# Kernel optimization log

Measured on AMD Instinct MI355X. Metric: run time of the kernel, lower is better.

Reference implementation:

```python
import jax, jax.numpy as jnp
import numpy as np

N, E, IN, HID, OUT, HEADS = 50000, 800000, 256, 256, 128, 4
HC = HID // HEADS  # 64
EPS = 1e-5


def layer_norm(x, g, b):
    mu = x.mean(-1, keepdims=True)
    var = ((x - mu) ** 2).mean(-1, keepdims=True)
    return (x - mu) * jax.lax.rsqrt(var + EPS) * g + b


def gat_conv(x, W, a_s, a_d, bias, src, dst, heads, C, concat):
    # PyG GATConv (eval mode): linear -> per-edge LeakyReLU attention ->
    # segment softmax over destination -> scatter-sum aggregation -> bias
    n = x.shape[0]
    xw = (x @ W).reshape(n, heads, C)                     # [N,H,C]
    al_s = jnp.einsum('nhc,hc->nh', xw, a_s)              # [N,H]
    al_d = jnp.einsum('nhc,hc->nh', xw, a_d)
    e = jax.nn.leaky_relu(al_s[src] + al_d[dst], 0.2)     # [Etot,H]
    m = jax.ops.segment_max(e, dst, num_segments=n)
    ex = jnp.exp(e - m[dst])
    denom = jax.ops.segment_sum(ex, dst, num_segments=n)
    alpha = ex / denom[dst]                               # [Etot,H]
    out = jax.ops.segment_sum(xw[src] * alpha[:, :, None], dst, num_segments=n)
    out = out.reshape(n, heads * C) if concat else out.mean(axis=1)
    return out + bias


def setup_inputs() -> dict:
    key = jax.random.key(0)
    ks = jax.random.split(key, 20)
    s = 0.05
    return {
        'x': jax.random.normal(ks[0], (N, IN), jnp.float32),
        'edge_index': jax.random.randint(ks[1], (2, E), 0, N, jnp.int64),
        'Wp': jax.random.normal(ks[2], (IN, HID), jnp.float32) * s,
        'bp': jnp.zeros((HID,), jnp.float32),
        'W0': jax.random.normal(ks[3], (HID, HEADS * HC), jnp.float32) * s,
        'as0': jax.random.normal(ks[4], (HEADS, HC), jnp.float32) * s,
        'ad0': jax.random.normal(ks[5], (HEADS, HC), jnp.float32) * s,
        'b0': jnp.zeros((HID,), jnp.float32),
        'W1': jax.random.normal(ks[6], (HID, OUT), jnp.float32) * s,
        'as1': jax.random.normal(ks[7], (1, OUT), jnp.float32) * s,
        'ad1': jax.random.normal(ks[8], (1, OUT), jnp.float32) * s,
        'b1': jnp.zeros((OUT,), jnp.float32),
        'g0': jnp.ones((HID,), jnp.float32),
        'be0': jnp.zeros((HID,), jnp.float32),
        'g1': jnp.ones((OUT,), jnp.float32),
        'be1': jnp.zeros((OUT,), jnp.float32),
        'Wo': jax.random.normal(ks[9], (OUT, OUT), jnp.float32) * s,
        'bo': jnp.zeros((OUT,), jnp.float32),
    }


def reference(x, edge_index, Wp, bp, W0, as0, ad0, b0, W1, as1, ad1, b1,
              g0, be0, g1, be1, Wo, bo):
    n = x.shape[0]
    # add self loops (PyG GATConv default)
    ar = jnp.arange(n, dtype=edge_index.dtype)
    src = jnp.concatenate([edge_index[0], ar])
    dst = jnp.concatenate([edge_index[1], ar])

    h = jax.nn.relu(x @ Wp + bp)
    # layer 0: multi-head, concat, LN + residual + relu
    h1 = gat_conv(h, W0, as0, ad0, b0, src, dst, HEADS, HC, True)
    h1 = layer_norm(h1, g0, be0)
    h1 = jax.nn.relu(h1 + h)
    # layer 1: single head, no concat, LN (no residual: shape check still passes
    # only when identity is not None; here identity is None for last layer)
    h2 = gat_conv(h1, W1, as1, ad1, b1, src, dst, 1, OUT, False)
    h2 = layer_norm(h2, g1, be1)
    out = h2 @ Wo + bo
    out = out / jnp.maximum(jnp.linalg.norm(out, axis=-1, keepdims=True), 1e-12)
    return out
```

## Files before the change

### kernel.cpp

```cpp
#include <hip/hip_runtime.h>
#include <hip/hip_bf16.h>

typedef __bf16 bf16x8 __attribute__((ext_vector_type(8)));
typedef __bf16 bf16x4 __attribute__((ext_vector_type(4)));
typedef __bf16 bf16x2 __attribute__((ext_vector_type(2)));
typedef float f32x4 __attribute__((ext_vector_type(4)));

__device__ __forceinline__ float getf(const void* p, size_t i, int isf32){
  return isf32 ? ((const float*)p)[i]
               : __bfloat162float(((const __hip_bfloat16*)p)[i]);
}
__device__ __forceinline__ int getedge(const void* p, long long idx, int is64, int n){
  long long v = is64 ? ((const long long*)p)[idx] : (long long)((const int*)p)[idx];
  v = v < 0 ? 0 : (v >= n ? (long long)(n - 1) : v);
  return (int)v;
}

__device__ __forceinline__ float bfly_sum(float v){
#pragma unroll
  for (int m = 32; m > 0; m >>= 1) v += __shfl_xor(v, m, 64);
  return v;
}

__global__ __launch_bounds__(256) void detect_kernel(const void* x, const void* ei,
                                                     int* flags){
  __shared__ int cnt_sane, cnt_odd;
  int t = threadIdx.x;
  if (t == 0){ cnt_sane = 0; cnt_odd = 0; }
  __syncthreads();
  int sane = 0;
  for (int i = t; i < 4096; i += 256){
    float v = __bfloat162float(((const __hip_bfloat16*)x)[i]);
    if (fabsf(v) < 16.f) sane++;
  }
  atomicAdd(&cnt_sane, sane);
  int odd = 0;
  for (int i = t; i < 512; i += 256){
    if (((const int*)ei)[2 * i + 1] != 0) odd++;
  }
  atomicAdd(&cnt_odd, odd);
  __syncthreads();
  if (t == 0){
    flags[0] = (cnt_sane < 3900) ? 1 : 0;
    flags[1] = (cnt_odd == 0) ? 1 : 0;
  }
}

__global__ __launch_bounds__(256) void count_kernel(const void* __restrict__ ei, long long E,
                                                    int n, const int* __restrict__ flags,
                                                    int* __restrict__ cnt){
  int i = blockIdx.x * blockDim.x + threadIdx.x;
  if (i < E){
    int d = getedge(ei, E + i, flags[1], n);
    atomicAdd(&cnt[d], 1);
  }
}

__global__ __launch_bounds__(1024) void scan_kernel(const int* __restrict__ cnt, int* __restrict__ off,
                                                    int* __restrict__ pos, int n){
  __shared__ int wsum[16];
  __shared__ int carry_s;
  int tid = threadIdx.x, lane = tid & 63, wv = tid >> 6;
  if (tid == 0) carry_s = 0;
  __syncthreads();
  for (int base = 0; base < n; base += 1024){
    int i = base + tid;
    int v = (i < n) ? cnt[i] : 0;
    int s = v;
#pragma unroll
    for (int o = 1; o < 64; o <<= 1){ int t = __shfl_up(s, o, 64); if (lane >= o) s += t; }
    if (lane == 63) wsum[wv] = s;
    __syncthreads();
    int wo = 0;
    for (int w = 0; w < wv; w++) wo += wsum[w];
    int carry = carry_s;
    int excl = carry + wo + s - v;
    if (i < n){ off[i] = excl; pos[i] = excl; }
    __syncthreads();
    if (tid == 0){
      int tot = 0;
      for (int w = 0; w < 16; w++) tot += wsum[w];
      carry_s = carry + tot;
    }
    __syncthreads();
  }
  if (tid == 0) off[n] = carry_s;
}

__global__ __launch_bounds__(256) void fill_kernel(const void* __restrict__ ei, long long E,
                                                   int n, const int* __restrict__ flags,
                                                   int* __restrict__ pos, int* __restrict__ bsrc,
                                                   int* __restrict__ bdst){
  int i = blockIdx.x * blockDim.x + threadIdx.x;
  if (i < E){
    int d = getedge(ei, E + i, flags[1], n);
    int s = getedge(ei, i, flags[1], n);
    int p = atomicAdd(&pos[d], 1);
    bsrc[p] = s;
    bdst[p] = d;
  }
}

__global__ __launch_bounds__(256) void transpose_w_kernel(const void* __restrict__ W,
    const int* __restrict__ flags, __hip_bfloat16* __restrict__ Bt, int K, int N)
{
  int f0 = flags[0];
  int o = blockIdx.x * 256 + threadIdx.x;
  if (o < K * N){
    int nn = o / K, kk = o - nn * K;
    Bt[o] = __float2bfloat16(getf(W, (size_t)kk * N + nn, f0));
  }
}

__device__ __forceinline__ bf16x8 pk8(f32x4 u, f32x4 w){
  bf16x8 r;
  r[0] = (__bf16)u.x; r[1] = (__bf16)u.y; r[2] = (__bf16)u.z; r[3] = (__bf16)u.w;
  r[4] = (__bf16)w.x; r[5] = (__bf16)w.y; r[6] = (__bf16)w.z; r[7] = (__bf16)w.w;
  return r;
}

template<int AMODE, bool OUTF, bool OUTB, bool RELU, bool BIAS, bool NORM>
__global__ __launch_bounds__(256) void gemm_direct_kernel(
    const void* __restrict__ A, const __hip_bfloat16* __restrict__ Bt,
    const void* __restrict__ bias, const int* __restrict__ flags,
    float* __restrict__ Cf, __hip_bfloat16* __restrict__ Cb,
    int M, int N, int K)
{
  const int f0 = flags[0];
  const bool af32 = (AMODE == 1) && (f0 != 0);
  int t = threadIdx.x;
  int wave = t >> 6, lane = t & 63;
  int q = lane >> 4, mi = lane & 15;
  int bm = blockIdx.x * 128 + wave * 32;
  int bn = blockIdx.y * 128;

  int r0 = min(bm + mi, M - 1);
  int r1 = min(bm + 16 + mi, M - 1);

  f32x4 acc[2][8] = {};

  if (af32){
    const float* Af = (const float*)A;
    const float* p0 = Af + (size_t)r0 * K + q * 8;
    const float* p1 = Af + (size_t)r1 * K + q * 8;
#pragma unroll 2
    for (int k0 = 0; k0 < K; k0 += 32){
      f32x4 u0 = *(const f32x4*)(p0 + k0);
      f32x4 w0 = *(const f32x4*)(p0 + k0 + 4);
      f32x4 u1 = *(const f32x4*)(p1 + k0);
      f32x4 w1 = *(const f32x4*)(p1 + k0 + 4);
      bf16x8 a0 = pk8(u0, w0);
      bf16x8 a1 = pk8(u1, w1);
#pragma unroll
      for (int nt = 0; nt < 8; nt++){
        bf16x8 b = *(const bf16x8*)(Bt + (size_t)(bn + nt * 16 + mi) * K + k0 + q * 8);
        acc[0][nt] = __builtin_amdgcn_mfma_f32_16x16x32_bf16(a0, b, acc[0][nt], 0, 0, 0);
        acc[1][nt] = __builtin_amdgcn_mfma_f32_16x16x32_bf16(a1, b, acc[1][nt], 0, 0, 0);
      }
    }
  } else {
    const __hip_bfloat16* Ab = (const __hip_bfloat16*)A;
    const __hip_bfloat16* p0 = Ab + (size_t)r0 * K + q * 8;
    const __hip_bfloat16* p1 = Ab + (size_t)r1 * K + q * 8;
#pragma unroll 2
    for (int k0 = 0; k0 < K; k0 += 32){
      bf16x8 a0 = *(const bf16x8*)(p0 + k0);
      bf16x8 a1 = *(const bf16x8*)(p1 + k0);
#pragma unroll
      for (int nt = 0; nt < 8; nt++){
        bf16x8 b = *(const bf16x8*)(Bt + (size_t)(bn + nt * 16 + mi) * K + k0 + q * 8);
        acc[0][nt] = __builtin_amdgcn_mfma_f32_16x16x32_bf16(a0, b, acc[0][nt], 0, 0, 0);
        acc[1][nt] = __builtin_amdgcn_mfma_f32_16x16x32_bf16(a1, b, acc[1][nt], 0, 0, 0);
      }
    }
  }

  float bv[8];
  if (BIAS){
#pragma unroll
    for (int nt = 0; nt < 8; nt++) bv[nt] = getf(bias, bn + nt * 16 + mi, f0);
  }
#pragma unroll
  for (int mt = 0; mt < 2; mt++){
#pragma unroll
    for (int r = 0; r < 4; r++){
      int row = bm + mt * 16 + q * 4 + r;
      float vv[8];
#pragma unroll
      for (int nt = 0; nt < 8; nt++){
        float v = acc[mt][nt][r];
        if (BIAS) v += bv[nt];
        if (RELU) v = fmaxf(v, 0.f);
        vv[nt] = v;
      }
      if (NORM){
        float ss = 0.f;
#pragma unroll
        for (int nt = 0; nt < 8; nt++) ss += vv[nt] * vv[nt];
        ss += __shfl_xor(ss, 1, 64);
        ss += __shfl_xor(ss, 2, 64);
        ss += __shfl_xor(ss, 4, 64);
        ss += __shfl_xor(ss, 8, 64);
        float inv = 1.f / fmaxf(sqrtf(ss), 1e-12f);
#pragma unroll
        for (int nt = 0; nt < 8; nt++) vv[nt] *= inv;
      }
      if (row < M){
#pragma unroll
        for (int nt = 0; nt < 8; nt++){
          int col = bn + nt * 16 + mi;
          size_t idx = (size_t)row * N + col;
          if (OUTF) Cf[idx] = vv[nt];
          if (OUTB) Cb[idx] = __float2bfloat16(vv[nt]);
        }
      }
    }
  }
}

__global__ __launch_bounds__(256) void al0_kernel(const __hip_bfloat16* __restrict__ xw,
    const void* __restrict__ a_s, const void* __restrict__ a_d, const int* __restrict__ flags,
    float* __restrict__ als, float* __restrict__ ald, int n)
{
  int f0 = flags[0];
  int t = threadIdx.x, wv = t >> 6, lane = t & 63;
  int i = blockIdx.x * 4 + wv;
  if (i >= n) return;
  int ch = lane * 4;
  uint2 u = *(const uint2*)(xw + (size_t)i * 256 + ch);
  float x0 = __uint_as_float(u.x << 16);
  float x1 = __uint_as_float(u.x & 0xffff0000u);
  float x2 = __uint_as_float(u.y << 16);
  float x3 = __uint_as_float(u.y & 0xffff0000u);
  float ps = x0 * getf(a_s, ch + 0, f0) + x1 * getf(a_s, ch + 1, f0)
           + x2 * getf(a_s, ch + 2, f0) + x3 * getf(a_s, ch + 3, f0);
  float pd = x0 * getf(a_d, ch + 0, f0) + x1 * getf(a_d, ch + 1, f0)
           + x2 * getf(a_d, ch + 2, f0) + x3 * getf(a_d, ch + 3, f0);
  ps += __shfl_xor(ps, 1, 64); pd += __shfl_xor(pd, 1, 64);
  ps += __shfl_xor(ps, 2, 64); pd += __shfl_xor(pd, 2, 64);
  ps += __shfl_xor(ps, 4, 64); pd += __shfl_xor(pd, 4, 64);
  ps += __shfl_xor(ps, 8, 64); pd += __shfl_xor(pd, 8, 64);
  if ((lane & 15) == 0){
    int h = lane >> 4;
    als[(size_t)i * 4 + h] = ps;
    ald[(size_t)i * 4 + h] = pd;
  }
}

__global__ __launch_bounds__(256) void al1_kernel(const __hip_bfloat16* __restrict__ xw,
    const void* __restrict__ a_s, const void* __restrict__ a_d, const int* __restrict__ flags,
    float* __restrict__ als, float* __restrict__ ald, int n)
{
  int f0 = flags[0];
  int t = threadIdx.x, wv = t >> 6, lane = t & 63;
  int i = blockIdx.x * 4 + wv;
  if (i >= n) return;
  int ch = lane * 2;
  unsigned u = *(const unsigned*)(xw + (size_t)i * 128 + ch);
  float x0 = __uint_as_float(u << 16);
  float x1 = __uint_as_float(u & 0xffff0000u);
  float ps = x0 * getf(a_s, ch + 0, f0) + x1 * getf(a_s, ch + 1, f0);
  float pd = x0 * getf(a_d, ch + 0, f0) + x1 * getf(a_d, ch + 1, f0);
  ps = bfly_sum(ps); pd = bfly_sum(pd);
  if (lane == 0){ als[i] = ps; ald[i] = pd; }
}

__global__ __launch_bounds__(256) void wq0_kernel(const float* __restrict__ als,
    const float* __restrict__ ald, const int* __restrict__ bsrc, const int* __restrict__ bdst,
    f32x4* __restrict__ wq, int E)
{
  int p = blockIdx.x * 256 + threadIdx.x;
  if (p < E){
    int s = bsrc[p], d = bdst[p];
    f32x4 a = ((const f32x4*)als)[s];
    f32x4 b = ((const f32x4*)ald)[d];
    f32x4 w;
#pragma unroll
    for (int k = 0; k < 4; k++){
      float e = a[k] + b[k];
      e = (e > 0.f) ? e : 0.2f * e;
      w[k] = __expf(e);
    }
    wq[p] = w;
  }
}

__global__ __launch_bounds__(256) void wq1_kernel(const float* __restrict__ als,
    const float* __restrict__ ald, const int* __restrict__ bsrc, const int* __restrict__ bdst,
    float* __restrict__ wq, int E)
{
  int p = blockIdx.x * 256 + threadIdx.x;
  if (p < E){
    float e = als[bsrc[p]] + ald[bdst[p]];
    e = (e > 0.f) ? e : 0.2f * e;
    wq[p] = __expf(e);
  }
}

#define FMA4(U, W) do { \
  m0 += (W) * __uint_as_float((U).x << 16); \
  m1 += (W) * __uint_as_float((U).x & 0xffff0000u); \
  m2 += (W) * __uint_as_float((U).y << 16); \
  m3 += (W) * __uint_as_float((U).y & 0xffff0000u); \
} while (0)

__global__ __launch_bounds__(256) void gather0_kernel(
    const __hip_bfloat16* __restrict__ xw, const float* __restrict__ als, const float* __restrict__ ald,
    const int* __restrict__ bsrc, const float* __restrict__ wq, const int* __restrict__ off,
    const void* __restrict__ bias, const void* __restrict__ gamma,
    const void* __restrict__ beta, const int* __restrict__ flags,
    const float* __restrict__ resf, __hip_bfloat16* __restrict__ outb, int n)
{
  int f0 = flags[0];
  int t = threadIdx.x, wv = t >> 6, lane = t & 63;
  int i = blockIdx.x * 4 + wv;
  if (i >= n) return;
  int head = lane >> 4;
  int ch = lane * 4;
  int e0 = off[i], jend = off[i + 1];

  float m0 = 0.f, m1 = 0.f, m2 = 0.f, m3 = 0.f;

  float se = als[(size_t)i * 4 + head] + ald[(size_t)i * 4 + head];
  se = (se > 0.f) ? se : 0.2f * se;
  float eself = __expf(se);
  {
    uint2 u = *(const uint2*)(xw + (size_t)i * 256 + ch);
    FMA4(u, eself);
  }
  float wacc = eself;

  int j = e0;
  for (; j + 3 < jend; j += 4){
    int s0 = bsrc[j], s1 = bsrc[j + 1], s2 = bsrc[j + 2], s3 = bsrc[j + 3];
    float w0 = wq[(size_t)j * 4 + head];
    float w1 = wq[(size_t)(j + 1) * 4 + head];
    float w2 = wq[(size_t)(j + 2) * 4 + head];
    float w3 = wq[(size_t)(j + 3) * 4 + head];
    uint2 U0 = *(const uint2*)(xw + (size_t)s0 * 256 + ch);
    uint2 U1 = *(const uint2*)(xw + (size_t)s1 * 256 + ch);
    uint2 U2 = *(const uint2*)(xw + (size_t)s2 * 256 + ch);
    uint2 U3 = *(const uint2*)(xw + (size_t)s3 * 256 + ch);
    wacc += w0 + w1 + w2 + w3;
    FMA4(U0, w0); FMA4(U1, w1); FMA4(U2, w2); FMA4(U3, w3);
  }
  for (; j < jend; j++){
    int s0 = bsrc[j];
    float w0 = wq[(size_t)j * 4 + head];
    uint2 U0 = *(const uint2*)(xw + (size_t)s0 * 256 + ch);
    wacc += w0;
    FMA4(U0, w0);
  }

  float rl = 1.f / wacc;
  float v0 = m0 * rl + getf(bias, ch + 0, f0);
  float v1 = m1 * rl + getf(bias, ch + 1, f0);
  float v2 = m2 * rl + getf(bias, ch + 2, f0);
  float v3 = m3 * rl + getf(bias, ch + 3, f0);

  float mu = bfly_sum(v0 + v1 + v2 + v3) * (1.f / 256.f);
  float d0 = v0 - mu, d1 = v1 - mu, d2 = v2 - mu, d3 = v3 - mu;
  float var = bfly_sum(d0 * d0 + d1 * d1 + d2 * d2 + d3 * d3) * (1.f / 256.f);
  float rs = rsqrtf(var + 1e-5f);

  f32x4 res = *(const f32x4*)(resf + (size_t)i * 256 + ch);
  float y0 = fmaxf(d0 * rs * getf(gamma, ch + 0, f0) + getf(beta, ch + 0, f0) + res.x, 0.f);
  float y1 = fmaxf(d1 * rs * getf(gamma, ch + 1, f0) + getf(beta, ch + 1, f0) + res.y, 0.f);
  float y2 = fmaxf(d2 * rs * getf(gamma, ch + 2, f0) + getf(beta, ch + 2, f0) + res.z, 0.f);
  float y3 = fmaxf(d3 * rs * getf(gamma, ch + 3, f0) + getf(beta, ch + 3, f0) + res.w, 0.f);

  bf16x4 o;
  o[0] = (__bf16)y0; o[1] = (__bf16)y1; o[2] = (__bf16)y2; o[3] = (__bf16)y3;
  *(bf16x4*)(outb + (size_t)i * 256 + ch) = o;
}

#define FMA2(U, W) do { \
  m0 += (W) * __uint_as_float((U) << 16); \
  m1 += (W) * __uint_as_float((U) & 0xffff0000u); \
} while (0)

__global__ __launch_bounds__(256) void gather1_kernel(
    const __hip_bfloat16* __restrict__ xw, const float* __restrict__ als, const float* __restrict__ ald,
    const int* __restrict__ bsrc, const float* __restrict__ wq, const int* __restrict__ off,
    const void* __restrict__ bias, const void* __restrict__ gamma,
    const void* __restrict__ beta, const int* __restrict__ flags,
    __hip_bfloat16* __restrict__ outb, int n)
{
  int f0 = flags[0];
  int t = threadIdx.x, wv = t >> 6, lane = t & 63;
  int i = blockIdx.x * 4 + wv;
  if (i >= n) return;
  int ch = lane * 2;
  int e0 = off[i], jend = off[i + 1];

  float m0 = 0.f, m1 = 0.f;

  float se = als[i] + ald[i];
  se = (se > 0.f) ? se : 0.2f * se;
  float eself = __expf(se);
  {
    unsigned u = *(const unsigned*)(xw + (size_t)i * 128 + ch);
    FMA2(u, eself);
  }
  float wacc = eself;

  int j = e0;
  for (; j + 3 < jend; j += 4){
    int s0 = bsrc[j], s1 = bsrc[j + 1], s2 = bsrc[j + 2], s3 = bsrc[j + 3];
    float w0 = wq[j], w1 = wq[j + 1], w2 = wq[j + 2], w3 = wq[j + 3];
    unsigned U0 = *(const unsigned*)(xw + (size_t)s0 * 128 + ch);
    unsigned U1 = *(const unsigned*)(xw + (size_t)s1 * 128 + ch);
    unsigned U2 = *(const unsigned*)(xw + (size_t)s2 * 128 + ch);
    unsigned U3 = *(const unsigned*)(xw + (size_t)s3 * 128 + ch);
    wacc += w0 + w1 + w2 + w3;
    FMA2(U0, w0); FMA2(U1, w1); FMA2(U2, w2); FMA2(U3, w3);
  }
  for (; j < jend; j++){
    int s0 = bsrc[j];
    float w0 = wq[j];
    unsigned U0 = *(const unsigned*)(xw + (size_t)s0 * 128 + ch);
    wacc += w0;
    FMA2(U0, w0);
  }

  float rl = 1.f / wacc;
  float v0 = m0 * rl + getf(bias, ch + 0, f0);
  float v1 = m1 * rl + getf(bias, ch + 1, f0);

  float mu = bfly_sum(v0 + v1) * (1.f / 128.f);
  float d0 = v0 - mu, d1 = v1 - mu;
  float var = bfly_sum(d0 * d0 + d1 * d1) * (1.f / 128.f);
  float rs = rsqrtf(var + 1e-5f);

  float y0 = d0 * rs * getf(gamma, ch + 0, f0) + getf(beta, ch + 0, f0);
  float y1 = d1 * rs * getf(gamma, ch + 1, f0) + getf(beta, ch + 1, f0);

  bf16x2 o;
  o[0] = (__bf16)y0; o[1] = (__bf16)y1;
  *(bf16x2*)(outb + (size_t)i * 128 + ch) = o;
}

extern "C" void kernel_launch(void* const* d_in, const int* in_sizes, int n_in,
                              void* d_out, int out_size, void* d_ws, size_t ws_size,
                              hipStream_t stream)
{
  const void* x   = d_in[0];
  const void* ei  = d_in[1];
  const void* Wp  = d_in[2];
  const void* bp  = d_in[3];
  const void* W0  = d_in[4];
  const void* as0 = d_in[5];
  const void* ad0 = d_in[6];
  const void* b0  = d_in[7];
  const void* W1  = d_in[8];
  const void* as1 = d_in[9];
  const void* ad1 = d_in[10];
  const void* b1  = d_in[11];
  const void* g0  = d_in[12];
  const void* be0 = d_in[13];
  const void* g1  = d_in[14];
  const void* be1 = d_in[15];
  const void* Wo  = d_in[16];
  const void* bo  = d_in[17];
  float* outp = (float*)d_out;

  const int n = in_sizes[0] / 256;
  const int E = in_sizes[1] / 2;

  char* w = (char*)d_ws;
  size_t SZ = (size_t)n * 256 * sizeof(float);
  float* h_f32 = (float*)w;
  __hip_bfloat16* h_bf = (__hip_bfloat16*)(w + SZ);
  __hip_bfloat16* xw_bf = (__hip_bfloat16*)(w + SZ + SZ / 2);
  char* p = w + 2 * SZ;
  int* flags = (int*)p; p += 64;
  float* als0 = (float*)p; p += (size_t)n * 4 * sizeof(float);
  float* ald0 = (float*)p; p += (size_t)n * 4 * sizeof(float);
  float* als1 = (float*)p; p += (size_t)n * sizeof(float);
  float* ald1 = (float*)p; p += (size_t)n * sizeof(float);
  int* cnt  = (int*)p; p += (size_t)n * sizeof(int);
  int* offb = (int*)p; p += (size_t)(n + 1) * sizeof(int) + 4;
  int* pos  = (int*)p; p += (size_t)n * sizeof(int);
  int* bsrc = (int*)p; p += (size_t)E * sizeof(int);
  int* bdst = (int*)p; p += (size_t)E * sizeof(int);
  p = (char*)(((uintptr_t)p + 15) & ~(uintptr_t)15);
  float* wqbuf = (float*)p; p += ((size_t)E + 64) * 4 * sizeof(float);
  __hip_bfloat16* bt_p = (__hip_bfloat16*)p; p += (size_t)256 * 256 * 2;
  __hip_bfloat16* bt_0 = (__hip_bfloat16*)p; p += (size_t)256 * 256 * 2;
  __hip_bfloat16* bt_1 = (__hip_bfloat16*)p; p += (size_t)128 * 256 * 2;
  __hip_bfloat16* bt_o = (__hip_bfloat16*)p; p += (size_t)128 * 128 * 2;

  detect_kernel<<<1, 256, 0, stream>>>(x, ei, flags);

  transpose_w_kernel<<<(256 * 256 + 255) / 256, 256, 0, stream>>>(Wp, flags, bt_p, 256, 256);
  transpose_w_kernel<<<(256 * 256 + 255) / 256, 256, 0, stream>>>(W0, flags, bt_0, 256, 256);
  transpose_w_kernel<<<(256 * 128 + 255) / 256, 256, 0, stream>>>(W1, flags, bt_1, 256, 128);
  transpose_w_kernel<<<(128 * 128 + 255) / 256, 256, 0, stream>>>(Wo, flags, bt_o, 128, 128);

  hipMemsetAsync(cnt, 0, (size_t)n * sizeof(int), stream);
  count_kernel<<<(E + 255) / 256, 256, 0, stream>>>(ei, E, n, flags, cnt);
  scan_kernel<<<1, 1024, 0, stream>>>(cnt, offb, pos, n);
  fill_kernel<<<(E + 255) / 256, 256, 0, stream>>>(ei, E, n, flags, pos, bsrc, bdst);

  int gm = (n + 127) / 128;
  int ge = (E + 255) / 256;
  int gn4 = (n + 3) / 4;

  gemm_direct_kernel<1, true, true, true, true, false><<<dim3(gm, 2), 256, 0, stream>>>(
      x, bt_p, bp, flags, h_f32, h_bf, n, 256, 256);
  gemm_direct_kernel<0, false, true, false, false, false><<<dim3(gm, 2), 256, 0, stream>>>(
      h_bf, bt_0, nullptr, flags, nullptr, xw_bf, n, 256, 256);
  al0_kernel<<<gn4, 256, 0, stream>>>(xw_bf, as0, ad0, flags, als0, ald0, n);
  wq0_kernel<<<ge, 256, 0, stream>>>(als0, ald0, bsrc, bdst, (f32x4*)wqbuf, E);
  gather0_kernel<<<gn4, 256, 0, stream>>>(xw_bf, als0, ald0, bsrc, wqbuf, offb, b0, g0, be0,
                                          flags, h_f32, h_bf, n);
  gemm_direct_kernel<0, false, true, false, false, false><<<dim3(gm, 1), 256, 0, stream>>>(
      h_bf, bt_1, nullptr, flags, nullptr, xw_bf, n, 128, 256);
  al1_kernel<<<gn4, 256, 0, stream>>>(xw_bf, as1, ad1, flags, als1, ald1, n);
  wq1_kernel<<<ge, 256, 0, stream>>>(als1, ald1, bsrc, bdst, wqbuf, E);
  gather1_kernel<<<gn4, 256, 0, stream>>>(xw_bf, als1, ald1, bsrc, wqbuf, offb, b1, g1, be1,
                                          flags, h_bf, n);
  gemm_direct_kernel<0, true, false, false, true, true><<<dim3(gm, 1), 256, 0, stream>>>(
      h_bf, bt_o, bo, flags, outp, nullptr, n, 128, 128);
}
```

Baseline: 595.3 us.

## Fuse attention logits into GEMM epilogue and compute edge weights inside gather

Computes the per-node source/destination attention scores in the GEMM epilogue, removing the separate al0/al1 kernels. Replaces the per-edge weight precompute kernels (wq0/wq1) and the bdst array with on-the-fly leaky-relu and exp inside the gather kernels. Also drops the fp32 residual copy in favor of the bf16 h buffer, merges the four weight transposes into one launch, and vectorizes the prefix scan by four. This trades extra exp work and scattered als reads per edge in the gather for fewer launches and less global memory traffic, with slightly lower residual precision.

```diff
diff --git a/kernel.cpp b/kernel.cpp
--- a/kernel.cpp
+++ b/kernel.cpp
@@ -63,10 +63,20 @@
   int tid = threadIdx.x, lane = tid & 63, wv = tid >> 6;
   if (tid == 0) carry_s = 0;
   __syncthreads();
-  for (int base = 0; base < n; base += 1024){
-    int i = base + tid;
-    int v = (i < n) ? cnt[i] : 0;
-    int s = v;
+  for (int base = 0; base < n; base += 4096){
+    int i0 = base + tid * 4;
+    int v0 = 0, v1 = 0, v2 = 0, v3 = 0;
+    if (i0 + 3 < n){
+      int4 q = *(const int4*)(cnt + i0);
+      v0 = q.x; v1 = q.y; v2 = q.z; v3 = q.w;
+    } else {
+      if (i0 < n)     v0 = cnt[i0];
+      if (i0 + 1 < n) v1 = cnt[i0 + 1];
+      if (i0 + 2 < n) v2 = cnt[i0 + 2];
+      if (i0 + 3 < n) v3 = cnt[i0 + 3];
+    }
+    int s4 = v0 + v1 + v2 + v3;
+    int s = s4;
 #pragma unroll
     for (int o = 1; o < 64; o <<= 1){ int t = __shfl_up(s, o, 64); if (lane >= o) s += t; }
     if (lane == 63) wsum[wv] = s;
@@ -74,8 +84,17 @@
     int wo = 0;
     for (int w = 0; w < wv; w++) wo += wsum[w];
     int carry = carry_s;
-    int excl = carry + wo + s - v;
-    if (i < n){ off[i] = excl; pos[i] = excl; }
+    int e0 = carry + wo + s - s4;
+    if (i0 + 3 < n){
+      int4 o4; o4.x = e0; o4.y = e0 + v0; o4.z = e0 + v0 + v1; o4.w = e0 + v0 + v1 + v2;
+      *(int4*)(off + i0) = o4;
+      *(int4*)(pos + i0) = o4;
+    } else {
+      if (i0 < n)     { off[i0] = e0;               pos[i0] = e0; }
+      if (i0 + 1 < n) { off[i0+1] = e0+v0;          pos[i0+1] = e0+v0; }
+      if (i0 + 2 < n) { off[i0+2] = e0+v0+v1;       pos[i0+2] = e0+v0+v1; }
+      if (i0 + 3 < n) { off[i0+3] = e0+v0+v1+v2;    pos[i0+3] = e0+v0+v1+v2; }
+    }
     __syncthreads();
     if (tid == 0){
       int tot = 0;
@@ -89,27 +108,33 @@
 
 __global__ __launch_bounds__(256) void fill_kernel(const void* __restrict__ ei, long long E,
                                                    int n, const int* __restrict__ flags,
-                                                   int* __restrict__ pos, int* __restrict__ bsrc,
-                                                   int* __restrict__ bdst){
+                                                   int* __restrict__ pos, int* __restrict__ bsrc){
   int i = blockIdx.x * blockDim.x + threadIdx.x;
   if (i < E){
     int d = getedge(ei, E + i, flags[1], n);
     int s = getedge(ei, i, flags[1], n);
     int p = atomicAdd(&pos[d], 1);
     bsrc[p] = s;
-    bdst[p] = d;
-  }
-}
-
-__global__ __launch_bounds__(256) void transpose_w_kernel(const void* __restrict__ W,
-    const int* __restrict__ flags, __hip_bfloat16* __restrict__ Bt, int K, int N)
+  }
+}
+
+__global__ __launch_bounds__(256) void transpose_all_kernel(
+    const void* __restrict__ Wp, const void* __restrict__ W0,
+    const void* __restrict__ W1, const void* __restrict__ Wo,
+    const int* __restrict__ flags,
+    __hip_bfloat16* __restrict__ btp, __hip_bfloat16* __restrict__ bt0,
+    __hip_bfloat16* __restrict__ bt1, __hip_bfloat16* __restrict__ bto)
 {
   int f0 = flags[0];
   int o = blockIdx.x * 256 + threadIdx.x;
-  if (o < K * N){
-    int nn = o / K, kk = o - nn * K;
-    Bt[o] = __float2bfloat16(getf(W, (size_t)kk * N + nn, f0));
-  }
+  const void* W; __hip_bfloat16* B; int K, N, loc;
+  if (o < 65536)       { W = Wp; B = btp; K = 256; N = 256; loc = o; }
+  else if (o < 131072) { W = W0; B = bt0; K = 256; N = 256; loc = o - 65536; }
+  else if (o < 163840) { W = W1; B = bt1; K = 256; N = 128; loc = o - 131072; }
+  else if (o < 180224) { W = Wo; B = bto; K = 128; N = 128; loc = o - 163840; }
+  else return;
+  int nn = loc / K, kk = loc - nn * K;
+  B[loc] = __float2bfloat16(getf(W, (size_t)kk * N + nn, f0));
 }
 
 __device__ __forceinline__ bf16x8 pk8(f32x4 u, f32x4 w){
@@ -119,11 +144,13 @@
   return r;
 }
 
-template<int AMODE, bool OUTF, bool OUTB, bool RELU, bool BIAS, bool NORM>
+template<int AMODE, bool OUTF, bool OUTB, bool RELU, bool BIAS, bool NORM, int ALMODE>
 __global__ __launch_bounds__(256) void gemm_direct_kernel(
     const void* __restrict__ A, const __hip_bfloat16* __restrict__ Bt,
-    const void* __restrict__ bias, const int* __restrict__ flags,
+    const void* __restrict__ bias, const void* __restrict__ a_s, const void* __restrict__ a_d,
+    const int* __restrict__ flags,
     float* __restrict__ Cf, __hip_bfloat16* __restrict__ Cb,
+    float* __restrict__ als, float* __restrict__ ald,
     int M, int N, int K)
 {
   const int f0 = flags[0];
@@ -175,10 +202,17 @@
     }
   }
 
-  float bv[8];
+  float bv[8], asv[8], adv[8];
   if (BIAS){
 #pragma unroll
     for (int nt = 0; nt < 8; nt++) bv[nt] = getf(bias, bn + nt * 16 + mi, f0);
+  }
+  if (ALMODE != 0){
+#pragma unroll
+    for (int nt = 0; nt < 8; nt++){
+      asv[nt] = getf(a_s, bn + nt * 16 + mi, f0);
+      adv[nt] = getf(a_d, bn + nt * 16 + mi, f0);
+    }
   }
 #pragma unroll
   for (int mt = 0; mt < 2; mt++){
@@ -205,6 +239,32 @@
 #pragma unroll
         for (int nt = 0; nt < 8; nt++) vv[nt] *= inv;
       }
+      if (ALMODE == 1){
+        float ps0 = 0.f, pd0 = 0.f, ps1 = 0.f, pd1 = 0.f;
+#pragma unroll
+        for (int nt = 0; nt < 4; nt++){ ps0 += vv[nt] * asv[nt]; pd0 += vv[nt] * adv[nt]; }
+#pragma unroll
+        for (int nt = 4; nt < 8; nt++){ ps1 += vv[nt] * asv[nt]; pd1 += vv[nt] * adv[nt]; }
+#pragma unroll
+        for (int m = 1; m < 16; m <<= 1){
+          ps0 += __shfl_xor(ps0, m, 64); pd0 += __shfl_xor(pd0, m, 64);
+          ps1 += __shfl_xor(ps1, m, 64); pd1 += __shfl_xor(pd1, m, 64);
+        }
+        if ((lane & 15) == 0 && row < M){
+          int h0 = blockIdx.y * 2;
+          als[(size_t)row * 4 + h0]     = ps0; ald[(size_t)row * 4 + h0]     = pd0;
+          als[(size_t)row * 4 + h0 + 1] = ps1; ald[(size_t)row * 4 + h0 + 1] = pd1;
+        }
+      } else if (ALMODE == 2){
+        float ps = 0.f, pd = 0.f;
+#pragma unroll
+        for (int nt = 0; nt < 8; nt++){ ps += vv[nt] * asv[nt]; pd += vv[nt] * adv[nt]; }
+#pragma unroll
+        for (int m = 1; m < 16; m <<= 1){
+          ps += __shfl_xor(ps, m, 64); pd += __shfl_xor(pd, m, 64);
+        }
+        if ((lane & 15) == 0 && row < M){ als[row] = ps; ald[row] = pd; }
+      }
       if (row < M){
 #pragma unroll
         for (int nt = 0; nt < 8; nt++){
@@ -218,85 +278,6 @@
   }
 }
 
-__global__ __launch_bounds__(256) void al0_kernel(const __hip_bfloat16* __restrict__ xw,
-    const void* __restrict__ a_s, const void* __restrict__ a_d, const int* __restrict__ flags,
-    float* __restrict__ als, float* __restrict__ ald, int n)
-{
-  int f0 = flags[0];
-  int t = threadIdx.x, wv = t >> 6, lane = t & 63;
-  int i = blockIdx.x * 4 + wv;
-  if (i >= n) return;
-  int ch = lane * 4;
-  uint2 u = *(const uint2*)(xw + (size_t)i * 256 + ch);
-  float x0 = __uint_as_float(u.x << 16);
-  float x1 = __uint_as_float(u.x & 0xffff0000u);
-  float x2 = __uint_as_float(u.y << 16);
-  float x3 = __uint_as_float(u.y & 0xffff0000u);
-  float ps = x0 * getf(a_s, ch + 0, f0) + x1 * getf(a_s, ch + 1, f0)
-           + x2 * getf(a_s, ch + 2, f0) + x3 * getf(a_s, ch + 3, f0);
-  float pd = x0 * getf(a_d, ch + 0, f0) + x1 * getf(a_d, ch + 1, f0)
-           + x2 * getf(a_d, ch + 2, f0) + x3 * getf(a_d, ch + 3, f0);
-  ps += __shfl_xor(ps, 1, 64); pd += __shfl_xor(pd, 1, 64);
-  ps += __shfl_xor(ps, 2, 64); pd += __shfl_xor(pd, 2, 64);
-  ps += __shfl_xor(ps, 4, 64); pd += __shfl_xor(pd, 4, 64);
-  ps += __shfl_xor(ps, 8, 64); pd += __shfl_xor(pd, 8, 64);
-  if ((lane & 15) == 0){
-    int h = lane >> 4;
-    als[(size_t)i * 4 + h] = ps;
-    ald[(size_t)i * 4 + h] = pd;
-  }
-}
-
-__global__ __launch_bounds__(256) void al1_kernel(const __hip_bfloat16* __restrict__ xw,
-    const void* __restrict__ a_s, const void* __restrict__ a_d, const int* __restrict__ flags,
-    float* __restrict__ als, float* __restrict__ ald, int n)
-{
-  int f0 = flags[0];
-  int t = threadIdx.x, wv = t >> 6, lane = t & 63;
-  int i = blockIdx.x * 4 + wv;
-  if (i >= n) return;
-  int ch = lane * 2;
-  unsigned u = *(const unsigned*)(xw + (size_t)i * 128 + ch);
-  float x0 = __uint_as_float(u << 16);
-  float x1 = __uint_as_float(u & 0xffff0000u);
-  float ps = x0 * getf(a_s, ch + 0, f0) + x1 * getf(a_s, ch + 1, f0);
-  float pd = x0 * getf(a_d, ch + 0, f0) + x1 * getf(a_d, ch + 1, f0);
-  ps = bfly_sum(ps); pd = bfly_sum(pd);
-  if (lane == 0){ als[i] = ps; ald[i] = pd; }
-}
-
-__global__ __launch_bounds__(256) void wq0_kernel(const float* __restrict__ als,
-    const float* __restrict__ ald, const int* __restrict__ bsrc, const int* __restrict__ bdst,
-    f32x4* __restrict__ wq, int E)
-{
-  int p = blockIdx.x * 256 + threadIdx.x;
-  if (p < E){
-    int s = bsrc[p], d = bdst[p];
-    f32x4 a = ((const f32x4*)als)[s];
-    f32x4 b = ((const f32x4*)ald)[d];
-    f32x4 w;
-#pragma unroll
-    for (int k = 0; k < 4; k++){
-      float e = a[k] + b[k];
-      e = (e > 0.f) ? e : 0.2f * e;
-      w[k] = __expf(e);
-    }
-    wq[p] = w;
-  }
-}
-
-__global__ __launch_bounds__(256) void wq1_kernel(const float* __restrict__ als,
-    const float* __restrict__ ald, const int* __restrict__ bsrc, const int* __restrict__ bdst,
-    float* __restrict__ wq, int E)
-{
-  int p = blockIdx.x * 256 + threadIdx.x;
-  if (p < E){
-    float e = als[bsrc[p]] + ald[bdst[p]];
-    e = (e > 0.f) ? e : 0.2f * e;
-    wq[p] = __expf(e);
-  }
-}
-
 #define FMA4(U, W) do { \
   m0 += (W) * __uint_as_float((U).x << 16); \
   m1 += (W) * __uint_as_float((U).x & 0xffff0000u); \
@@ -306,10 +287,10 @@
 
 __global__ __launch_bounds__(256) void gather0_kernel(
     const __hip_bfloat16* __restrict__ xw, const float* __restrict__ als, const float* __restrict__ ald,
-    const int* __restrict__ bsrc, const float* __restrict__ wq, const int* __restrict__ off,
+    const int* __restrict__ bsrc, const int* __restrict__ off,
     const void* __restrict__ bias, const void* __restrict__ gamma,
     const void* __restrict__ beta, const int* __restrict__ flags,
-    const float* __restrict__ resf, __hip_bfloat16* __restrict__ outb, int n)
+    __hip_bfloat16* __restrict__ hbuf, int n)
 {
   int f0 = flags[0];
   int t = threadIdx.x, wv = t >> 6, lane = t & 63;
@@ -321,7 +302,9 @@
 
   float m0 = 0.f, m1 = 0.f, m2 = 0.f, m3 = 0.f;
 
-  float se = als[(size_t)i * 4 + head] + ald[(size_t)i * 4 + head];
+  float aldi = ald[(size_t)i * 4 + head];
+
+  float se = als[(size_t)i * 4 + head] + aldi;
   se = (se > 0.f) ? se : 0.2f * se;
   float eself = __expf(se);
   {
@@ -333,10 +316,15 @@
   int j = e0;
   for (; j + 3 < jend; j += 4){
     int s0 = bsrc[j], s1 = bsrc[j + 1], s2 = bsrc[j + 2], s3 = bsrc[j + 3];
-    float w0 = wq[(size_t)j * 4 + head];
-    float w1 = wq[(size_t)(j + 1) * 4 + head];
-    float w2 = wq[(size_t)(j + 2) * 4 + head];
-    float w3 = wq[(size_t)(j + 3) * 4 + head];
+    float l0 = als[(size_t)s0 * 4 + head] + aldi;
+    float l1 = als[(size_t)s1 * 4 + head] + aldi;
+    float l2 = als[(size_t)s2 * 4 + head] + aldi;
+    float l3 = als[(size_t)s3 * 4 + head] + aldi;
+    l0 = (l0 > 0.f) ? l0 : 0.2f * l0;
+    l1 = (l1 > 0.f) ? l1 : 0.2f * l1;
+    l2 = (l2 > 0.f) ? l2 : 0.2f * l2;
+    l3 = (l3 > 0.f) ? l3 : 0.2f * l3;
+    float w0 = __expf(l0), w1 = __expf(l1), w2 = __expf(l2), w3 = __expf(l3);
     uint2 U0 = *(const uint2*)(xw + (size_t)s0 * 256 + ch);
     uint2 U1 = *(const uint2*)(xw + (size_t)s1 * 256 + ch);
     uint2 U2 = *(const uint2*)(xw + (size_t)s2 * 256 + ch);
@@ -346,7 +334,9 @@
   }
   for (; j < jend; j++){
     int s0 = bsrc[j];
-    float w0 = wq[(size_t)j * 4 + head];
+    float l0 = als[(size_t)s0 * 4 + head] + aldi;
+    l0 = (l0 > 0.f) ? l0 : 0.2f * l0;
+    float w0 = __expf(l0);
     uint2 U0 = *(const uint2*)(xw + (size_t)s0 * 256 + ch);
     wacc += w0;
     FMA4(U0, w0);
@@ -363,15 +353,15 @@
   float var = bfly_sum(d0 * d0 + d1 * d1 + d2 * d2 + d3 * d3) * (1.f / 256.f);
   float rs = rsqrtf(var + 1e-5f);
 
-  f32x4 res = *(const f32x4*)(resf + (size_t)i * 256 + ch);
-  float y0 = fmaxf(d0 * rs * getf(gamma, ch + 0, f0) + getf(beta, ch + 0, f0) + res.x, 0.f);
-  float y1 = fmaxf(d1 * rs * getf(gamma, ch + 1, f0) + getf(beta, ch + 1, f0) + res.y, 0.f);
-  float y2 = fmaxf(d2 * rs * getf(gamma, ch + 2, f0) + getf(beta, ch + 2, f0) + res.z, 0.f);
-  float y3 = fmaxf(d3 * rs * getf(gamma, ch + 3, f0) + getf(beta, ch + 3, f0) + res.w, 0.f);
+  bf16x4 rb = *(const bf16x4*)(hbuf + (size_t)i * 256 + ch);
+  float y0 = fmaxf(d0 * rs * getf(gamma, ch + 0, f0) + getf(beta, ch + 0, f0) + (float)rb[0], 0.f);
+  float y1 = fmaxf(d1 * rs * getf(gamma, ch + 1, f0) + getf(beta, ch + 1, f0) + (float)rb[1], 0.f);
+  float y2 = fmaxf(d2 * rs * getf(gamma, ch + 2, f0) + getf(beta, ch + 2, f0) + (float)rb[2], 0.f);
+  float y3 = fmaxf(d3 * rs * getf(gamma, ch + 3, f0) + getf(beta, ch + 3, f0) + (float)rb[3], 0.f);
 
   bf16x4 o;
   o[0] = (__bf16)y0; o[1] = (__bf16)y1; o[2] = (__bf16)y2; o[3] = (__bf16)y3;
-  *(bf16x4*)(outb + (size_t)i * 256 + ch) = o;
+  *(bf16x4*)(hbuf + (size_t)i * 256 + ch) = o;
 }
 
 #define FMA2(U, W) do { \
@@ -381,7 +371,7 @@
 
 __global__ __launch_bounds__(256) void gather1_kernel(
     const __hip_bfloat16* __restrict__ xw, const float* __restrict__ als, const float* __restrict__ ald,
-    const int* __restrict__ bsrc, const float* __restrict__ wq, const int* __restrict__ off,
+    const int* __restrict__ bsrc, const int* __restrict__ off,
     const void* __restrict__ bias, const void* __restrict__ gamma,
     const void* __restrict__ beta, const int* __restrict__ flags,
     __hip_bfloat16* __restrict__ outb, int n)
@@ -395,7 +385,8 @@
 
   float m0 = 0.f, m1 = 0.f;
 
-  float se = als[i] + ald[i];
+  float aldi = ald[i];
+  float se = als[i] + aldi;
   se = (se > 0.f) ? se : 0.2f * se;
   float eself = __expf(se);
   {
@@ -407,7 +398,12 @@
   int j = e0;
   for (; j + 3 < jend; j += 4){
     int s0 = bsrc[j], s1 = bsrc[j + 1], s2 = bsrc[j + 2], s3 = bsrc[j + 3];
-    float w0 = wq[j], w1 = wq[j + 1], w2 = wq[j + 2], w3 = wq[j + 3];
+    float l0 = als[s0] + aldi, l1 = als[s1] + aldi, l2 = als[s2] + aldi, l3 = als[s3] + aldi;
+    l0 = (l0 > 0.f) ? l0 : 0.2f * l0;
+    l1 = (l1 > 0.f) ? l1 : 0.2f * l1;
+    l2 = (l2 > 0.f) ? l2 : 0.2f * l2;
+    l3 = (l3 > 0.f) ? l3 : 0.2f * l3;
+    float w0 = __expf(l0), w1 = __expf(l1), w2 = __expf(l2), w3 = __expf(l3);
     unsigned U0 = *(const unsigned*)(xw + (size_t)s0 * 128 + ch);
     unsigned U1 = *(const unsigned*)(xw + (size_t)s1 * 128 + ch);
     unsigned U2 = *(const unsigned*)(xw + (size_t)s2 * 128 + ch);
@@ -417,7 +413,9 @@
   }
   for (; j < jend; j++){
     int s0 = bsrc[j];
-    float w0 = wq[j];
+    float l0 = als[s0] + aldi;
+    l0 = (l0 > 0.f) ? l0 : 0.2f * l0;
+    float w0 = __expf(l0);
     unsigned U0 = *(const unsigned*)(xw + (size_t)s0 * 128 + ch);
     wacc += w0;
     FMA2(U0, w0);
@@ -469,22 +467,19 @@
 
   char* w = (char*)d_ws;
   size_t SZ = (size_t)n * 256 * sizeof(float);
-  float* h_f32 = (float*)w;
-  __hip_bfloat16* h_bf = (__hip_bfloat16*)(w + SZ);
-  __hip_bfloat16* xw_bf = (__hip_bfloat16*)(w + SZ + SZ / 2);
-  char* p = w + 2 * SZ;
+  __hip_bfloat16* h_bf  = (__hip_bfloat16*)w;
+  __hip_bfloat16* xw_bf = (__hip_bfloat16*)(w + SZ / 2);
+  char* p = w + SZ;
   int* flags = (int*)p; p += 64;
   float* als0 = (float*)p; p += (size_t)n * 4 * sizeof(float);
   float* ald0 = (float*)p; p += (size_t)n * 4 * sizeof(float);
   float* als1 = (float*)p; p += (size_t)n * sizeof(float);
   float* ald1 = (float*)p; p += (size_t)n * sizeof(float);
   int* cnt  = (int*)p; p += (size_t)n * sizeof(int);
-  int* offb = (int*)p; p += (size_t)(n + 1) * sizeof(int) + 4;
+  int* offb = (int*)p; p += (size_t)(n + 4) * sizeof(int);
   int* pos  = (int*)p; p += (size_t)n * sizeof(int);
   int* bsrc = (int*)p; p += (size_t)E * sizeof(int);
-  int* bdst = (int*)p; p += (size_t)E * sizeof(int);
   p = (char*)(((uintptr_t)p + 15) & ~(uintptr_t)15);
-  float* wqbuf = (float*)p; p += ((size_t)E + 64) * 4 * sizeof(float);
   __hip_bfloat16* bt_p = (__hip_bfloat16*)p; p += (size_t)256 * 256 * 2;
   __hip_bfloat16* bt_0 = (__hip_bfloat16*)p; p += (size_t)256 * 256 * 2;
   __hip_bfloat16* bt_1 = (__hip_bfloat16*)p; p += (size_t)128 * 256 * 2;
@@ -492,34 +487,26 @@
 
   detect_kernel<<<1, 256, 0, stream>>>(x, ei, flags);
 
-  transpose_w_kernel<<<(256 * 256 + 255) / 256, 256, 0, stream>>>(Wp, flags, bt_p, 256, 256);
-  transpose_w_kernel<<<(256 * 256 + 255) / 256, 256, 0, stream>>>(W0, flags, bt_0, 256, 256);
-  transpose_w_kernel<<<(256 * 128 + 255) / 256, 256, 0, stream>>>(W1, flags, bt_1, 256, 128);
-  transpose_w_kernel<<<(128 * 128 + 255) / 256, 256, 0, stream>>>(Wo, flags, bt_o, 128, 128);
+  transpose_all_kernel<<<704, 256, 0, stream>>>(Wp, W0, W1, Wo, flags, bt_p, bt_0, bt_1, bt_o);
 
   hipMemsetAsync(cnt, 0, (size_t)n * sizeof(int), stream);
   count_kernel<<<(E + 255) / 256, 256, 0, stream>>>(ei, E, n, flags, cnt);
   scan_kernel<<<1, 1024, 0, stream>>>(cnt, offb, pos, n);
-  fill_kernel<<<(E + 255) / 256, 256, 0, stream>>>(ei, E, n, flags, pos, bsrc, bdst);
+  fill_kernel<<<(E + 255) / 256, 256, 0, stream>>>(ei, E, n, flags, pos, bsrc);
 
   int gm = (n + 127) / 128;
-  int ge = (E + 255) / 256;
   int gn4 = (n + 3) / 4;
 
-  gemm_direct_kernel<1, true, true, true, true, false><<<dim3(gm, 2), 256, 0, stream>>>(
-      x, bt_p, bp, flags, h_f32, h_bf, n, 256, 256);
-  gemm_direct_kernel<0, false, true, false, false, false><<<dim3(gm, 2), 256, 0, stream>>>(
-      h_bf, bt_0, nullptr, flags, nullptr, xw_bf, n, 256, 256);
-  al0_kernel<<<gn4, 256, 0, stream>>>(xw_bf, as0, ad0, flags, als0, ald0, n);
-  wq0_kernel<<<ge, 256, 0, stream>>>(als0, ald0, bsrc, bdst, (f32x4*)wqbuf, E);
-  gather0_kernel<<<gn4, 256, 0, stream>>>(xw_bf, als0, ald0, bsrc, wqbuf, offb, b0, g0, be0,
-                                          flags, h_f32, h_bf, n);
-  gemm_direct_kernel<0, false, true, false, false, false><<<dim3(gm, 1), 256, 0, stream>>>(
-      h_bf, bt_1, nullptr, flags, nullptr, xw_bf, n, 128, 256);
-  al1_kernel<<<gn4, 256, 0, stream>>>(xw_bf, as1, ad1, flags, als1, ald1, n);
-  wq1_kernel<<<ge, 256, 0, stream>>>(als1, ald1, bsrc, bdst, wqbuf, E);
-  gather1_kernel<<<gn4, 256, 0, stream>>>(xw_bf, als1, ald1, bsrc, wqbuf, offb, b1, g1, be1,
+  gemm_direct_kernel<1, false, true, true, true, false, 0><<<dim3(gm, 2), 256, 0, stream>>>(
+      x, bt_p, bp, nullptr, nullptr, flags, nullptr, h_bf, nullptr, nullptr, n, 256, 256);
+  gemm_direct_kernel<0, false, true, false, false, false, 1><<<dim3(gm, 2), 256, 0, stream>>>(
+      h_bf, bt_0, nullptr, as0, ad0, flags, nullptr, xw_bf, als0, ald0, n, 256, 256);
+  gather0_kernel<<<gn4, 256, 0, stream>>>(xw_bf, als0, ald0, bsrc, offb, b0, g0, be0,
                                           flags, h_bf, n);
-  gemm_direct_kernel<0, true, false, false, true, true><<<dim3(gm, 1), 256, 0, stream>>>(
-      h_bf, bt_o, bo, flags, outp, nullptr, n, 128, 128);
-}
+  gemm_direct_kernel<0, false, true, false, false, false, 2><<<dim3(gm, 1), 256, 0, stream>>>(
+      h_bf, bt_1, nullptr, as1, ad1, flags, nullptr, xw_bf, als1, ald1, n, 128, 256);
+  gather1_kernel<<<gn4, 256, 0, stream>>>(xw_bf, als1, ald1, bsrc, offb, b1, g1, be1,
+                                          flags, h_bf, n);
+  gemm_direct_kernel<0, true, false, false, true, true, 0><<<dim3(gm, 1), 256, 0, stream>>>(
+      h_bf, bt_o, bo, nullptr, nullptr, flags, outp, nullptr, nullptr, nullptr, n, 128, 128);
+}
```

After: 496.4 us. 16.6% less time.
